# Kernel tuning notes

Measured on AMD Instinct MI355X. Metric: run time of the kernel, lower is better.

## Reference

```python
import jax, jax.numpy as jnp
import numpy as np

V, D, K, B = 100000, 300, 200, 256


def setup_inputs() -> dict:
    key = jax.random.key(0)
    k1, k2, k3, k4, k5 = jax.random.split(key, 5)
    word_vectors = jax.random.normal(k1, (V, D), dtype=jnp.float32)
    mu = jax.random.normal(k2, (K, D), dtype=jnp.float32)
    cov_factor = jax.random.normal(k3, (K, D), dtype=jnp.float32)  # rank-1 factor, trailing dim squeezed
    cov_diag = jnp.clip(jax.random.uniform(k4, (K, D), dtype=jnp.float32) * 50.0, 1e-6)
    sampled_x = jax.random.normal(k5, (B, K), dtype=jnp.float32)
    return {"sampled_x": sampled_x, "word_vectors": word_vectors, "mu": mu,
            "cov_factor": cov_factor, "cov_diag": cov_diag}


def reference(sampled_x, word_vectors, mu, cov_factor, cov_diag):
    # Rank-1 LowRankMultivariateNormal log-prob via Sherman-Morrison / Woodbury.
    # cov_k = w_k w_k^T + diag(D_k);  x: (V, d) broadcast against K topics.
    d = word_vectors.shape[1]
    Dinv = 1.0 / cov_diag                                        # (K, d)
    cap = 1.0 + jnp.sum(cov_factor * cov_factor * Dinv, axis=1)  # (K,) capacitance scalar
    logdet = jnp.sum(jnp.log(cov_diag), axis=1) + jnp.log(cap)   # (K,)
    u = cov_factor * Dinv                                        # (K, d) = D^{-1} w
    # quadratic form diff^T D^{-1} diff, expanded to avoid a (V, K, d) intermediate
    q = (jnp.square(word_vectors) @ Dinv.T
         - 2.0 * (word_vectors @ (mu * Dinv).T)
         + jnp.sum(jnp.square(mu) * Dinv, axis=1))               # (V, K)
    t = word_vectors @ u.T - jnp.sum(mu * u, axis=1)             # (V, K) = diff^T D^{-1} w
    mahalanobis = q - jnp.square(t) / cap                        # (V, K)
    log2pi = jnp.float32(np.log(2.0 * np.pi))
    logp = -0.5 * (d * log2pi + logdet + mahalanobis)            # (V, K)
    topic_word_dist = jax.nn.softmax(logp.T, axis=-1)            # (K, V)
    word_dist = sampled_x @ topic_word_dist                      # (B, V)
    return jnp.concatenate([sampled_x, word_dist], axis=1)       # (B, K + V)
```

## Files before the change

kernel.cpp:

```cpp
#include <hip/hip_runtime.h>
#include <math.h>

#define V_N 100000
#define D_N 300
#define K_N 200
#define B_N 256

#define SC 128.0f
#define SC_INV 0.0078125f

typedef _Float16 h4 __attribute__((ext_vector_type(4)));
typedef _Float16 h8 __attribute__((ext_vector_type(8)));
typedef float f4v __attribute__((ext_vector_type(4)));

typedef __attribute__((address_space(1))) const void gvoid;
typedef __attribute__((address_space(3))) void lvoid;

static constexpr size_t P_OFF     = 0;
static constexpr size_t CB_OFF    = (size_t)K_N * V_N;
static constexpr size_t ALPHA_OFF = CB_OFF + 225280;
static constexpr size_t S_OFF     = ALPHA_OFF + 256;
static constexpr size_t HIC_OFF   = S_OFF + 256;
static constexpr size_t M_OFF     = HIC_OFF + 256;
static constexpr size_t Z_OFF     = M_OFF + 256;
static constexpr size_t PM_OFF    = Z_OFF + 256;
static constexpr size_t PS_OFF    = PM_OFF + 800;
static constexpr size_t YF_OFF    = CB_OFF;

__global__ __launch_bounds__(256) void topic_prep(
    const float* __restrict__ mu, const float* __restrict__ w,
    const float* __restrict__ diag,
    float* __restrict__ alpha, float* __restrict__ sArr,
    float* __restrict__ hic)
{
    int k = blockIdx.x;
    int tid = threadIdx.x;
    if (k >= K_N) {
        if (tid == 0) { alpha[k] = 0.f; sArr[k] = 0.f; hic[k] = 0.f; }
        return;
    }
    float capp = 0.f, logd = 0.f, cpart = 0.f, spart = 0.f;
    for (int d = tid; d < D_N; d += 256) {
        float Dg = diag[k * D_N + d];
        float Di = 1.0f / Dg;
        float wvv = w[k * D_N + d];
        float m  = mu[k * D_N + d];
        float u  = wvv * Di;
        capp  += wvv * u;
        logd  += logf(Dg);
        cpart += m * m * Di;
        spart += m * u;
    }
    __shared__ float4 red[256];
    red[tid] = make_float4(capp, logd, cpart, spart);
    __syncthreads();
    for (int s = 128; s > 0; s >>= 1) {
        if (tid < s) {
            float4 a = red[tid], b = red[tid + s];
            red[tid] = make_float4(a.x + b.x, a.y + b.y, a.z + b.z, a.w + b.w);
        }
        __syncthreads();
    }
    if (tid == 0) {
        float4 r = red[0];
        float cap = 1.0f + r.x;
        float logdet = r.y + logf(cap);
        const float LOG2PI = 1.8378770664093453f;
        alpha[k] = -0.5f * ((float)D_N * LOG2PI + logdet + r.z);
        sArr[k]  = r.w;
        hic[k]   = 0.5f / cap;
    }
}

__global__ __launch_bounds__(256) void coef_prep(
    const float* __restrict__ mu, const float* __restrict__ w,
    const float* __restrict__ cd, _Float16* __restrict__ cB)
{
    int id = blockIdx.x * 256 + threadIdx.x;
    if (id >= 450560) return;
    int chunk = id / 22528;
    int rem   = id % 22528;
    int kb = chunk / 10, c = chunk % 10;
    _Float16 outv = (_Float16)0.f;
    if (rem < 21504) {
        int arr = rem / 3584;
        int r2  = rem % 3584;
        int n = r2 >> 5;
        int h = r2 & 31;
        int p = h >> 3, r = h & 7;
        int q = (p - (n >> 1)) & 3;
        int d = c * 32 + q * 8 + r;
        int topic = kb * 112 + n;
        if (topic < K_N && d < D_N) {
            float Di = 1.0f / cd[topic * D_N + d];
            float val;
            if (arr < 2)      val = -0.5f * Di * SC_INV;
            else if (arr < 4) val = mu[topic * D_N + d] * Di * SC_INV;
            else              val = w[topic * D_N + d] * Di * SC_INV;
            _Float16 hi = (_Float16)val;
            outv = (arr & 1) ? (_Float16)(val - (float)hi) : hi;
        }
    }
    cB[id] = outv;
}

__global__ __launch_bounds__(256, 2) void logp_mfma(
    const float* __restrict__ wv, const _Float16* __restrict__ cB,
    const float* __restrict__ alphaA, const float* __restrict__ sA,
    const float* __restrict__ hA, float* __restrict__ P)
{
    __shared__ _Float16 smem[38912];
    _Float16* As = smem;
    _Float16* Bs = smem + 16384;

    const int tid = threadIdx.x;
    const int kb = blockIdx.x;
    const int v0 = blockIdx.y * 128;
    const int lane = tid & 63;
    const int quad = lane >> 4, lr = lane & 15;
    const int wm = (tid >> 6) * 32;
    const int dq = tid & 7, vr = tid >> 3;

    f4v C1[2][7], C2[2][7];
    #pragma unroll
    for (int i = 0; i < 2; ++i)
        #pragma unroll
        for (int j = 0; j < 7; ++j) {
            C1[i][j] = (f4v){0.f, 0.f, 0.f, 0.f};
            C2[i][j] = (f4v){0.f, 0.f, 0.f, 0.f};
        }

    const int row0 = wm + lr, row1 = wm + 16 + lr;
    const int pA = (quad + (row0 >> 1)) & 3;
    const int offA0 = row0 * 32 + pA * 8;
    const int offA1 = row1 * 32 + pA * 8;

    for (int c = 0; c < 10; ++c) {
        __syncthreads();
        {
            const _Float16* slab = cB + (size_t)(kb * 10 + c) * 22528 + tid * 8;
            _Float16* dst = Bs + tid * 8;
            #pragma unroll
            for (int it = 0; it < 11; ++it) {
                __builtin_amdgcn_global_load_lds(
                    (gvoid*)(slab + it * 2048), (lvoid*)(dst + it * 2048),
                    16, 0, 0);
            }
        }
        const int d0 = c * 32;
        #pragma unroll
        for (int rep = 0; rep < 4; ++rep) {
            int v = vr + rep * 32;
            int gv = v0 + v;
            int d = d0 + dq * 4;
            float4 a = make_float4(0.f, 0.f, 0.f, 0.f);
            if (gv < V_N && d < D_N)
                a = *(const float4*)(wv + (size_t)gv * D_N + d);
            float av[4] = {a.x, a.y, a.z, a.w};
            h4 ah, al, qh, ql;
            #pragma unroll
            for (int j = 0; j < 4; ++j) {
                float x = av[j];
                _Float16 xh = (_Float16)x;
                ah[j] = xh;
                al[j] = (_Float16)(x - (float)xh);
                float xs = x * x;
                _Float16 sh = (_Float16)xs;
                qh[j] = sh;
                ql[j] = (_Float16)(xs - (float)sh);
            }
            int p = ((dq >> 1) + (v >> 1)) & 3;
            int base = v * 32 + p * 8 + (dq & 1) * 4;
            *(h4*)(As + 0 * 4096 + base) = qh;
            *(h4*)(As + 1 * 4096 + base) = ql;
            *(h4*)(As + 2 * 4096 + base) = ah;
            *(h4*)(As + 3 * 4096 + base) = al;
        }
        __syncthreads();

        h8 fqh0 = *(const h8*)(As + 0 * 4096 + offA0);
        h8 fqh1 = *(const h8*)(As + 0 * 4096 + offA1);
        h8 fql0 = *(const h8*)(As + 1 * 4096 + offA0);
        h8 fql1 = *(const h8*)(As + 1 * 4096 + offA1);
        h8 fah0 = *(const h8*)(As + 2 * 4096 + offA0);
        h8 fah1 = *(const h8*)(As + 2 * 4096 + offA1);
        h8 fal0 = *(const h8*)(As + 3 * 4096 + offA0);
        h8 fal1 = *(const h8*)(As + 3 * 4096 + offA1);

        h8 bf[7];
        #define LDB(arr)                                                       \
            _Pragma("unroll")                                                  \
            for (int nt = 0; nt < 7; ++nt) {                                   \
                int n = nt * 16 + lr;                                          \
                bf[nt] = *(const h8*)(Bs + (arr) * 3584 + n * 32               \
                                      + (((quad + (n >> 1)) & 3) << 3));       \
            }
        #define MF(ACC, MT, FR)                                                \
            _Pragma("unroll")                                                  \
            for (int nt = 0; nt < 7; ++nt)                                     \
                ACC[MT][nt] = __builtin_amdgcn_mfma_f32_16x16x32_f16(          \
                    FR, bf[nt], ACC[MT][nt], 0, 0, 0);

        LDB(0)
        MF(C1, 0, fqh0) MF(C1, 1, fqh1) MF(C1, 0, fql0) MF(C1, 1, fql1)
        LDB(1)
        MF(C1, 0, fqh0) MF(C1, 1, fqh1)
        LDB(2)
        MF(C1, 0, fah0) MF(C1, 1, fah1) MF(C1, 0, fal0) MF(C1, 1, fal1)
        LDB(3)
        MF(C1, 0, fah0) MF(C1, 1, fah1)
        LDB(4)
        MF(C2, 0, fah0) MF(C2, 1, fah1) MF(C2, 0, fal0) MF(C2, 1, fal1)
        LDB(5)
        MF(C2, 0, fah0) MF(C2, 1, fah1)
        #undef LDB
        #undef MF
    }

    __syncthreads();
    float* Ct = (float*)smem;
    #pragma unroll
    for (int nt = 0; nt < 7; ++nt) {
        int nl = nt * 16 + lr;
        int ng = kb * 112 + nl;
        float al = alphaA[ng], sk = sA[ng], hk = hA[ng];
        #pragma unroll
        for (int mt = 0; mt < 2; ++mt) {
            f4v c1 = C1[mt][nt], c2 = C2[mt][nt];
            f4v res;
            #pragma unroll
            for (int r = 0; r < 4; ++r) {
                float t = SC * c2[r] - sk;
                res[r] = al + SC * c1[r] + hk * t * t;
            }
            *(f4v*)(Ct + nl * 132 + wm + mt * 16 + quad * 4) = res;
        }
    }
    __syncthreads();
    #pragma unroll
    for (int i = 0; i < 14; ++i) {
        int id = tid + i * 256;
        int m4 = (id & 31) * 4;
        int nl = id >> 5;
        int kg = kb * 112 + nl;
        if (kg < K_N) {
            f4v val = *(const f4v*)(Ct + nl * 132 + m4);
            int v = v0 + m4;
            if (v + 3 < V_N) {
                *(float4*)(P + (size_t)kg * V_N + v) =
                    make_float4(val[0], val[1], val[2], val[3]);
            } else {
                for (int j = 0; j < 4; ++j)
                    if (v + j < V_N) P[(size_t)kg * V_N + v + j] = val[j];
            }
        }
    }
}

__global__ __launch_bounds__(256) void softmax_stats(
    const float* __restrict__ P, float* __restrict__ pm,
    float* __restrict__ ps)
{
    int k = blockIdx.x >> 2, part = blockIdx.x & 3;
    int tid = threadIdx.x;
    const float4* row = (const float4*)(P + (size_t)k * V_N) + part * 6250;
    float m = -INFINITY, s = 0.f;
    for (int i = tid; i < 6250; i += 256) {
        float4 x = row[i];
        float mx = fmaxf(fmaxf(x.x, x.y), fmaxf(x.z, x.w));
        if (mx > m) { s *= __expf(m - mx); m = mx; }
        s += __expf(x.x - m) + __expf(x.y - m)
           + __expf(x.z - m) + __expf(x.w - m);
    }
    __shared__ float ms[256], ss[256];
    ms[tid] = m; ss[tid] = s;
    __syncthreads();
    for (int off = 128; off > 0; off >>= 1) {
        if (tid < off) {
            float mo = ms[tid], so = ss[tid];
            float m2 = ms[tid + off], s2 = ss[tid + off];
            float mn = fmaxf(mo, m2);
            ms[tid] = mn;
            ss[tid] = so * __expf(mo - mn) + s2 * __expf(m2 - mn);
        }
        __syncthreads();
    }
    if (tid == 0) { pm[blockIdx.x] = ms[0]; ps[blockIdx.x] = ss[0]; }
}

__global__ __launch_bounds__(256) void stats_merge(
    const float* __restrict__ pm, const float* __restrict__ ps,
    float* __restrict__ mArr, float* __restrict__ zArr)
{
    int k = threadIdx.x;
    if (k < K_N) {
        float m = -INFINITY, s = 0.f;
        #pragma unroll
        for (int p = 0; p < 4; ++p) {
            float m2 = pm[k * 4 + p], s2 = ps[k * 4 + p];
            float mn = fmaxf(m, m2);
            s = s * __expf(m - mn) + s2 * __expf(m2 - mn);
            m = mn;
        }
        mArr[k] = m; zArr[k] = s;
    }
}

__global__ __launch_bounds__(256) void prep_y(
    const float* __restrict__ x, const float* __restrict__ zArr,
    _Float16* __restrict__ yF, float* __restrict__ out)
{
    int id = blockIdx.x * 256 + threadIdx.x;
    if (id < 57344) {
        int j = id & 7;
        int b = (id >> 3) & 255;
        int q = (id >> 11) & 3;
        int kc = id >> 13;
        int k = kc * 32 + q * 8 + j;
        float v = 0.f;
        if (k < K_N) v = x[b * K_N + k] / zArr[k];
        yF[id] = (_Float16)v;
    } else {
        int id2 = id - 57344;
        if (id2 < B_N * K_N) {
            int b = id2 / K_N, k = id2 % K_N;
            out[(size_t)b * (K_N + V_N) + k] = x[id2];
        }
    }
}

__global__ __launch_bounds__(256) void out_gemm(
    const float* __restrict__ P, const _Float16* __restrict__ yF,
    const float* __restrict__ mArr, float* __restrict__ out)
{
    __shared__ float Es[32][134];

    const int tid = threadIdx.x;
    const int b0 = blockIdx.x * 64;
    const int v0 = blockIdx.y * 128;
    const int lane = tid & 63;
    const int quad = lane >> 4, lr = lane & 15;
    const int wm = (tid >> 6) * 32;

    f4v acc[2][4];
    #pragma unroll
    for (int i = 0; i < 2; ++i)
        #pragma unroll
        for (int j = 0; j < 4; ++j) acc[i][j] = (f4v){0.f, 0.f, 0.f, 0.f};

    const int kr = tid >> 3;
    const int vq = tid & 7;

    for (int kc = 0; kc < 7; ++kc) {
        __syncthreads();
        int k = kc * 32 + kr;
        bool kok = k < K_N;
        float mk = kok ? mArr[k] : 0.f;
        #pragma unroll
        for (int i = 0; i < 4; ++i) {
            int vv = (vq + i * 8) * 4;
            float4 pv;
            if (kok && v0 + vv + 3 < V_N) {
                pv = *(const float4*)(P + (size_t)k * V_N + v0 + vv);
                pv = make_float4(pv.x - mk, pv.y - mk, pv.z - mk, pv.w - mk);
            } else {
                pv = make_float4(-1e30f, -1e30f, -1e30f, -1e30f);
            }
            *(float2*)&Es[kr][vv]     = make_float2(pv.x, pv.y);
            *(float2*)&Es[kr][vv + 2] = make_float2(pv.z, pv.w);
        }
        __syncthreads();

        h8 yf[4];
        #pragma unroll
        for (int nt = 0; nt < 4; ++nt)
            yf[nt] = *(const h8*)(yF + (((size_t)(kc * 4 + quad) * 256)
                                        + b0 + nt * 16 + lr) * 8);

        #pragma unroll
        for (int mt = 0; mt < 2; ++mt) {
            int row = wm + mt * 16 + lr;
            h8 af;
            #pragma unroll
            for (int j = 0; j < 8; ++j)
                af[j] = (_Float16)__expf(Es[quad * 8 + j][row]);
            #pragma unroll
            for (int nt = 0; nt < 4; ++nt)
                acc[mt][nt] = __builtin_amdgcn_mfma_f32_16x16x32_f16(
                    af, yf[nt], acc[mt][nt], 0, 0, 0);
        }
    }

    #pragma unroll
    for (int mt = 0; mt < 2; ++mt) {
        int v = v0 + wm + mt * 16 + quad * 4;
        #pragma unroll
        for (int nt = 0; nt < 4; ++nt) {
            int b = b0 + nt * 16 + lr;
            float* dst = out + (size_t)b * (K_N + V_N) + K_N + v;
            f4v a = acc[mt][nt];
            if (v + 3 < V_N) {
                *(float4*)dst = make_float4(a[0], a[1], a[2], a[3]);
            } else {
                for (int j = 0; j < 4; ++j)
                    if (v + j < V_N) dst[j] = a[j];
            }
        }
    }
}

extern "C" void kernel_launch(void* const* d_in, const int* in_sizes, int n_in,
                              void* d_out, int out_size, void* d_ws, size_t ws_size,
                              hipStream_t stream) {
    const float* x    = (const float*)d_in[0];
    const float* wv   = (const float*)d_in[1];
    const float* mu   = (const float*)d_in[2];
    const float* cw   = (const float*)d_in[3];
    const float* cd   = (const float*)d_in[4];
    float* out = (float*)d_out;
    float* ws  = (float*)d_ws;

    float* P      = ws + P_OFF;
    _Float16* cB  = (_Float16*)(ws + CB_OFF);
    float* alpha  = ws + ALPHA_OFF;
    float* sArr   = ws + S_OFF;
    float* hic    = ws + HIC_OFF;
    float* mArr   = ws + M_OFF;
    float* zArr   = ws + Z_OFF;
    float* pm     = ws + PM_OFF;
    float* ps     = ws + PS_OFF;
    _Float16* yF  = (_Float16*)(ws + YF_OFF);

    topic_prep<<<256, 256, 0, stream>>>(mu, cw, cd, alpha, sArr, hic);
    coef_prep<<<1760, 256, 0, stream>>>(mu, cw, cd, cB);

    dim3 gB(2, (V_N + 127) / 128);
    logp_mfma<<<gB, 256, 0, stream>>>(wv, cB, alpha, sArr, hic, P);

    softmax_stats<<<K_N * 4, 256, 0, stream>>>(P, pm, ps);
    stats_merge<<<1, 256, 0, stream>>>(pm, ps, mArr, zArr);
    prep_y<<<(57344 + B_N * K_N + 255) / 256, 256, 0, stream>>>(x, zArr, yF, out);

    dim3 gD(4, (V_N + 127) / 128);
    out_gemm<<<gD, 256, 0, stream>>>(P, yF, mArr, out);
}
```

Baseline: 459.8 us.

## Retile output GEMM to cover all batch rows per block with LDS-staged y

The output GEMM block now covers all 256 batch rows and 64 vocab entries instead of 64x128. Each P element is therefore exponentiated once rather than four times across batch blocks, and P is read once instead of four times. The y operand for each k-chunk is staged into LDS with async global-to-LDS loads, which adds LDS traffic and 16 accumulator tiles per thread. The higher register pressure may lower occupancy.

After: 437.4 us. 4.9% less time.

```diff
diff --git a/kernel.cpp b/kernel.cpp
--- a/kernel.cpp
+++ b/kernel.cpp
@@ -333,31 +333,39 @@
     const float* __restrict__ P, const _Float16* __restrict__ yF,
     const float* __restrict__ mArr, float* __restrict__ out)
 {
-    __shared__ float Es[32][134];
+    __shared__ float Es[32][66];
+    __shared__ _Float16 Ys[8192];
 
     const int tid = threadIdx.x;
-    const int b0 = blockIdx.x * 64;
-    const int v0 = blockIdx.y * 128;
+    const int v0 = blockIdx.x * 64;
     const int lane = tid & 63;
     const int quad = lane >> 4, lr = lane & 15;
-    const int wm = (tid >> 6) * 32;
-
-    f4v acc[2][4];
+    const int w = tid >> 6;
+    const int row = w * 16 + lr;
+
+    f4v acc[16];
     #pragma unroll
-    for (int i = 0; i < 2; ++i)
-        #pragma unroll
-        for (int j = 0; j < 4; ++j) acc[i][j] = (f4v){0.f, 0.f, 0.f, 0.f};
+    for (int i = 0; i < 16; ++i) acc[i] = (f4v){0.f, 0.f, 0.f, 0.f};
 
     const int kr = tid >> 3;
     const int vq = tid & 7;
 
     for (int kc = 0; kc < 7; ++kc) {
         __syncthreads();
+        {
+            const _Float16* src = yF + (size_t)kc * 8192 + tid * 8;
+            _Float16* dst = Ys + tid * 8;
+            #pragma unroll
+            for (int it = 0; it < 4; ++it)
+                __builtin_amdgcn_global_load_lds(
+                    (gvoid*)(src + it * 2048), (lvoid*)(dst + it * 2048),
+                    16, 0, 0);
+        }
         int k = kc * 32 + kr;
         bool kok = k < K_N;
         float mk = kok ? mArr[k] : 0.f;
         #pragma unroll
-        for (int i = 0; i < 4; ++i) {
+        for (int i = 0; i < 2; ++i) {
             int vv = (vq + i * 8) * 4;
             float4 pv;
             if (kok && v0 + vv + 3 < V_N) {
@@ -371,40 +379,33 @@
         }
         __syncthreads();
 
-        h8 yf[4];
-        #pragma unroll
-        for (int nt = 0; nt < 4; ++nt)
-            yf[nt] = *(const h8*)(yF + (((size_t)(kc * 4 + quad) * 256)
-                                        + b0 + nt * 16 + lr) * 8);
-
-        #pragma unroll
-        for (int mt = 0; mt < 2; ++mt) {
-            int row = wm + mt * 16 + lr;
-            h8 af;
-            #pragma unroll
-            for (int j = 0; j < 8; ++j)
-                af[j] = (_Float16)__expf(Es[quad * 8 + j][row]);
-            #pragma unroll
-            for (int nt = 0; nt < 4; ++nt)
-                acc[mt][nt] = __builtin_amdgcn_mfma_f32_16x16x32_f16(
-                    af, yf[nt], acc[mt][nt], 0, 0, 0);
-        }
-    }
-
+        h8 yf[16];
+        #pragma unroll
+        for (int nt = 0; nt < 16; ++nt)
+            yf[nt] = *(const h8*)(Ys + ((size_t)(quad * 256) + nt * 16 + lr) * 8);
+
+        h8 af;
+        #pragma unroll
+        for (int j = 0; j < 8; ++j)
+            af[j] = (_Float16)__expf(Es[quad * 8 + j][row]);
+
+        #pragma unroll
+        for (int nt = 0; nt < 16; ++nt)
+            acc[nt] = __builtin_amdgcn_mfma_f32_16x16x32_f16(
+                af, yf[nt], acc[nt], 0, 0, 0);
+    }
+
+    int v = v0 + w * 16 + quad * 4;
     #pragma unroll
-    for (int mt = 0; mt < 2; ++mt) {
-        int v = v0 + wm + mt * 16 + quad * 4;
-        #pragma unroll
-        for (int nt = 0; nt < 4; ++nt) {
-            int b = b0 + nt * 16 + lr;
-            float* dst = out + (size_t)b * (K_N + V_N) + K_N + v;
-            f4v a = acc[mt][nt];
-            if (v + 3 < V_N) {
-                *(float4*)dst = make_float4(a[0], a[1], a[2], a[3]);
-            } else {
-                for (int j = 0; j < 4; ++j)
-                    if (v + j < V_N) dst[j] = a[j];
-            }
+    for (int nt = 0; nt < 16; ++nt) {
+        int b = nt * 16 + lr;
+        float* dst = out + (size_t)b * (K_N + V_N) + K_N + v;
+        f4v a = acc[nt];
+        if (v + 3 < V_N) {
+            *(float4*)dst = make_float4(a[0], a[1], a[2], a[3]);
+        } else {
+            for (int j = 0; j < 4; ++j)
+                if (v + j < V_N) dst[j] = a[j];
         }
     }
 }
@@ -441,6 +442,5 @@
     stats_merge<<<1, 256, 0, stream>>>(pm, ps, mArr, zArr);
     prep_y<<<(57344 + B_N * K_N + 255) / 256, 256, 0, stream>>>(x, zArr, yF, out);
 
-    dim3 gD(4, (V_N + 127) / 128);
-    out_gemm<<<gD, 256, 0, stream>>>(P, yF, mArr, out);
-}
+    out_gemm<<<(V_N + 63) / 64, 256, 0, stream>>>(P, yF, mArr, out);
+}
```
